# Kernel tuning notes

Hardware: AMD Instinct MI355X
Metric: run time of the kernel (lower is better)

Reference implementation:

```python
import jax, jax.numpy as jnp
import numpy as np


def _build_constants():
    # All 512 3x3 binary neighborhood patterns, flattened row-major; center = index 4.
    masks = np.array([[int(b) for b in f'{n:09b}'] for n in range(512)], dtype=np.float32)  # [512, 9]
    total = masks.sum(axis=1)
    alive = masks[:, 4] == 1.0
    # Game of Life: center alive next iff (alive and total in {3,4}) or (dead and total == 3)
    future = (alive & ((total == 3) | (total == 4))) | (~alive & (total == 3))
    msel = masks[future]  # [C=140, 9] alive-future patterns
    s = msel.sum(axis=1)
    # Inclusion-exclusion pairs: pattern i3 has 3 live cells, i4 has 4, and i3 is a subset of i4.
    union = ((msel[:, None, :] + msel[None, :, :]) > 0).sum(axis=-1)  # [C, C]
    pair = ((s[:, None] == 3.0) & (s[None, :] == 4.0) & (union == 4)).astype(np.float32)
    np.fill_diagonal(pair, 0.0)
    return jnp.asarray(msel), jnp.asarray(pair)


_MSEL, _PAIR = _build_constants()


def setup_inputs() -> dict:
    key = jax.random.key(0)
    B, H, W = 8, 256, 256
    x = jax.random.uniform(key, (B, 1, H, W), dtype=jnp.float32)  # per-cell alive probabilities
    return {"x": x}


def reference(x) -> jnp.ndarray:
    msel, pair = _MSEL, _PAIR  # [C, 9], [C, C]
    B, _, H, W = x.shape
    C = msel.shape[0]
    xb = x[:, 0]  # [B, H, W]
    # Circularly gather the 9 neighbors of each pixel (kernel position k -> offset (k//3 - 1, k%3 - 1)).
    neigh = jnp.stack(
        [jnp.roll(xb, (1 - k // 3, 1 - k % 3), axis=(1, 2)) for k in range(9)], axis=1
    ).reshape(B, 9, H * W)  # [B, 9, HW]
    # Per-pattern match probability: prod_k (n_k if mask bit else 1 - n_k)  (masked sign flip).
    acc = jnp.ones((B, C, H * W), dtype=x.dtype)
    for k in range(9):
        mk = msel[:, k][None, :, None]        # [1, C, 1]
        nk = neigh[:, k][:, None, :]          # [B, 1, HW]
        acc = acc * (mk * nk + (1.0 - mk) * (1.0 - nk))
    # Pairwise inclusion-exclusion correction over the selected pattern pairs.
    or_probs = jnp.einsum('bip,ij,bjp->bp', acc, pair, acc)  # [B, HW]
    prob = acc.sum(axis=1) - or_probs  # [B, HW]
    return prob.reshape(B, 1, H, W)
```

## Files before the change

### kernel.cpp

```cpp
#include <hip/hip_runtime.h>


__global__ __launch_bounds__(256)
void golr_kernel(const float* __restrict__ x, float* __restrict__ out) {
    constexpr int W = 256;
    constexpr int H = 256;
    const int row = blockIdx.x & (H - 1);
    const int b   = blockIdx.x >> 8;
    const int tx  = threadIdx.x;

    __shared__ float sh[3][W];

    const float* img = x + (size_t)b * H * W;
    const int ym = (row + H - 1) & (H - 1);
    const int yp = (row + 1) & (H - 1);

    sh[0][tx] = img[ym  * W + tx];
    sh[1][tx] = img[row * W + tx];
    sh[2][tx] = img[yp  * W + tx];
    __syncthreads();

    const int xm = (tx + W - 1) & (W - 1);
    const int xp = (tx + 1) & (W - 1);

    float n[9];
    n[0] = sh[0][xm]; n[1] = sh[0][tx]; n[2] = sh[0][xp];
    n[3] = sh[1][xm]; n[4] = sh[1][tx]; n[5] = sh[1][xp];
    n[6] = sh[2][xm]; n[7] = sh[2][tx]; n[8] = sh[2][xp];

    const float a = n[4];

    float c0 = 1.f, c1 = 0.f, c2 = 0.f, c3 = 0.f;
    float d00 = 1.f, d10 = 0.f, d20 = 0.f, d30 = 0.f;
    float d01 = 0.f, d11 = 0.f, d21 = 0.f;

#pragma unroll
    for (int k = 0; k < 9; ++k) {
        if (k == 4) continue;
        const float p  = n[k];
        const float np_ = 1.f - p;

        c3 = c3 * np_ + c2 * p;
        c2 = c2 * np_ + c1 * p;
        c1 = c1 * np_ + c0 * p;
        c0 = c0 * np_;

        const float q = p * p;
        const float r = np_ * np_;
        const float w = p * np_;

        d21 = d21 * r + d11 * q + d20 * w;
        d11 = d11 * r + d01 * q + d10 * w;
        d01 = d01 * r + d00 * w;
        d30 = d30 * r + d20 * q;
        d20 = d20 * r + d10 * q;
        d10 = d10 * r + d00 * q;
        d00 = d00 * r;
    }

    const float main_ = a * c2 + c3;
    const float wc = a * (1.f - a);
    const float qc = a * a;
    const float corr = wc * d30 + qc * d21;

    out[(size_t)b * H * W + row * W + tx] = main_ - corr;
}

extern "C" void kernel_launch(void* const* d_in, const int* in_sizes, int n_in,
                              void* d_out, int out_size, void* d_ws, size_t ws_size,
                              hipStream_t stream) {
    const float* x = (const float*)d_in[0];
    float* out = (float*)d_out;
    golr_kernel<<<dim3(2048), dim3(256), 0, stream>>>(x, out);
}
```

Before: 10.20 us.

## Compute four pixels per thread and four rows per block with vectorized IO

Each block now handles four rows, loading a six-row halo with float4 loads, and each thread computes four adjacent output pixels and stores them as one float4. The squared-probability DP is replaced by a 7-term elementary symmetric polynomial recurrence, with the pair correction expressed algebraically from those coefficients. This cuts redundant halo loads and raises per-thread work and memory-access width. The trade-offs are a quarter as many blocks, which lowers parallelism on a tiny problem, and a different floating-point formula for the correction.

```diff
diff --git a/kernel.cpp b/kernel.cpp
--- a/kernel.cpp
+++ b/kernel.cpp
@@ -3,67 +3,70 @@
 
 __global__ __launch_bounds__(256)
 void golr_kernel(const float* __restrict__ x, float* __restrict__ out) {
-    constexpr int W = 256;
-    constexpr int H = 256;
-    const int row = blockIdx.x & (H - 1);
-    const int b   = blockIdx.x >> 8;
-    const int tx  = threadIdx.x;
+    constexpr int W = 256, H = 256, R = 4;
+    const int blk = blockIdx.x;
+    const int b   = blk >> 6;
+    const int rowbase = (blk & 63) * R;
+    const int t    = threadIdx.x;
+    const int wave = t >> 6;
+    const int lane = t & 63;
 
-    __shared__ float sh[3][W];
+    __shared__ float sh[6][W];
 
     const float* img = x + (size_t)b * H * W;
-    const int ym = (row + H - 1) & (H - 1);
-    const int yp = (row + 1) & (H - 1);
 
-    sh[0][tx] = img[ym  * W + tx];
-    sh[1][tx] = img[row * W + tx];
-    sh[2][tx] = img[yp  * W + tx];
+    for (int i = t; i < 6 * 64; i += 256) {
+        const int ri = i >> 6, ci = i & 63;
+        const int grow = (rowbase - 1 + ri + H) & (H - 1);
+        ((float4*)sh[ri])[ci] = ((const float4*)(img + grow * W))[ci];
+    }
     __syncthreads();
 
-    const int xm = (tx + W - 1) & (W - 1);
-    const int xp = (tx + 1) & (W - 1);
+    const int c0i = lane * 4;
+    const int liX = (c0i + W - 1) & (W - 1);
+    const int riX = (c0i + 4) & (W - 1);
 
-    float n[9];
-    n[0] = sh[0][xm]; n[1] = sh[0][tx]; n[2] = sh[0][xp];
-    n[3] = sh[1][xm]; n[4] = sh[1][tx]; n[5] = sh[1][xp];
-    n[6] = sh[2][xm]; n[7] = sh[2][tx]; n[8] = sh[2][xp];
-
-    const float a = n[4];
-
-    float c0 = 1.f, c1 = 0.f, c2 = 0.f, c3 = 0.f;
-    float d00 = 1.f, d10 = 0.f, d20 = 0.f, d30 = 0.f;
-    float d01 = 0.f, d11 = 0.f, d21 = 0.f;
-
+    float a6[3][6];
 #pragma unroll
-    for (int k = 0; k < 9; ++k) {
-        if (k == 4) continue;
-        const float p  = n[k];
-        const float np_ = 1.f - p;
-
-        c3 = c3 * np_ + c2 * p;
-        c2 = c2 * np_ + c1 * p;
-        c1 = c1 * np_ + c0 * p;
-        c0 = c0 * np_;
-
-        const float q = p * p;
-        const float r = np_ * np_;
-        const float w = p * np_;
-
-        d21 = d21 * r + d11 * q + d20 * w;
-        d11 = d11 * r + d01 * q + d10 * w;
-        d01 = d01 * r + d00 * w;
-        d30 = d30 * r + d20 * q;
-        d20 = d20 * r + d10 * q;
-        d10 = d10 * r + d00 * q;
-        d00 = d00 * r;
+    for (int r = 0; r < 3; ++r) {
+        const float* row = sh[wave + r];
+        const float4 v = ((const float4*)row)[lane];
+        a6[r][0] = row[liX];
+        a6[r][1] = v.x; a6[r][2] = v.y; a6[r][3] = v.z; a6[r][4] = v.w;
+        a6[r][5] = row[riX];
     }
 
-    const float main_ = a * c2 + c3;
-    const float wc = a * (1.f - a);
-    const float qc = a * a;
-    const float corr = wc * d30 + qc * d21;
+    float o[4];
+#pragma unroll
+    for (int j = 0; j < 4; ++j) {
+        float p8[8];
+        p8[0] = a6[0][j]; p8[1] = a6[0][j + 1]; p8[2] = a6[0][j + 2];
+        p8[3] = a6[1][j];                       p8[4] = a6[1][j + 2];
+        p8[5] = a6[2][j]; p8[6] = a6[2][j + 1]; p8[7] = a6[2][j + 2];
+        const float a = a6[1][j + 1];
 
-    out[(size_t)b * H * W + row * W + tx] = main_ - corr;
+        float c0 = 1.f, c1 = 0.f, c2 = 0.f, c3 = 0.f, c4 = 0.f, c5 = 0.f, c6 = 0.f;
+#pragma unroll
+        for (int k = 0; k < 8; ++k) {
+            const float p = p8[k], np_ = 1.f - p;
+            c6 = c6 * np_ + c5 * p;
+            c5 = c5 * np_ + c4 * p;
+            c4 = c4 * np_ + c3 * p;
+            c3 = c3 * np_ + c2 * p;
+            c2 = c2 * np_ + c1 * p;
+            c1 = c1 * np_ + c0 * p;
+            c0 = c0 * np_;
+        }
+        const float E3q  = c3 * c3 - 2.f * (c6 * c0 - c5 * c1 + c4 * c2);
+        const float G    = 5.f * (c5 * c0) - 3.f * (c4 * c1) + c3 * c2;
+        const float mn   = a * c2 + c3;
+        const float corr = (a - a * a) * E3q + (a * a) * G;
+        o[j] = mn - corr;
+    }
+
+    float4 ov;
+    ov.x = o[0]; ov.y = o[1]; ov.z = o[2]; ov.w = o[3];
+    ((float4*)(out + (size_t)b * H * W + (size_t)(rowbase + wave) * W))[lane] = ov;
 }
 
 extern "C" void kernel_launch(void* const* d_in, const int* in_sizes, int n_in,
@@ -71,5 +74,5 @@
                               hipStream_t stream) {
     const float* x = (const float*)d_in[0];
     float* out = (float*)d_out;
-    golr_kernel<<<dim3(2048), dim3(256), 0, stream>>>(x, out);
+    golr_kernel<<<dim3(512), dim3(256), 0, stream>>>(x, out);
 }
```

New measurement: 9.959 us. 1.02x faster.
